# Optimization experiments

Hardware: AMD Instinct MI355X
Metric: run time of the kernel (lower is better)

Reference implementation:

```python
import jax, jax.numpy as jnp
import numpy as np

EPS = 1e-8


def setup_inputs() -> dict:
    key = jax.random.key(0)
    kx, kw, kb = jax.random.split(key, 3)
    B, S, K, N = 64, 4096, 256, 256
    x = jax.random.normal(kx, (B, S, K), dtype=jnp.float32)
    # Kaiming-uniform-ish init for weight (out_features, in_features)
    bound_w = np.sqrt(6.0 / K) / np.sqrt(1.0 + 5.0)  # kaiming_uniform with a=sqrt(5)
    weight = jax.random.uniform(kw, (N, K), dtype=jnp.float32, minval=-bound_w, maxval=bound_w)
    bound_b = 1.0 / np.sqrt(K)
    bias = jax.random.uniform(kb, (N,), dtype=jnp.float32, minval=-bound_b, maxval=bound_b)
    return {"x": x, "weight": weight, "bias": bias}


def reference(x, weight, bias):
    """LNS inference path of LNSLinear.

    log_out[m, n] = logsumexp_k(log(|x[m,k]|+eps) + log(|w[n,k]|+eps))
    out = sign(sign(x) @ sign(w).T) * exp(log_out) + bias
    Computed stably as log(exp(lx - mx) @ exp(lw - mw).T) + mx + mw.
    """
    orig_shape = x.shape
    K = weight.shape[1]
    xf = x.reshape(-1, K)                                  # [M, K]
    log_x = jnp.log(jnp.abs(xf) + EPS)                     # [M, K]
    x_sign = jnp.sign(xf)                                  # [M, K]
    log_w = jnp.log(jnp.abs(weight) + EPS)                 # [N, K]
    w_sign = jnp.sign(weight)                              # [N, K]

    mx = jnp.max(log_x, axis=-1, keepdims=True)            # [M, 1]
    mw = jnp.max(log_w, axis=-1, keepdims=True)            # [N, 1]
    # logsumexp over k without materializing [M, N, K]
    acc = jnp.einsum('mk,nk->mn', jnp.exp(log_x - mx), jnp.exp(log_w - mw))
    log_out = jnp.log(acc) + mx + mw.T                     # [M, N]

    out_sign = jnp.sign(jnp.einsum('mk,nk->mn', x_sign, w_sign))
    out = out_sign * jnp.exp(log_out) + bias
    return out.reshape(orig_shape[:-1] + (weight.shape[0],))
```

## Files before the change

### kernel.cpp

```cpp
#include <hip/hip_runtime.h>
#include <stdint.h>


#define K_DIM 256
#define N_DIM 256
#define BM 64
#define BN 128
#define BK 32
#define NKBLK 8
#define AROW 72

typedef float f32x4 __attribute__((ext_vector_type(4)));
typedef __bf16 bf16x8 __attribute__((ext_vector_type(8)));
typedef unsigned short u16x4v __attribute__((ext_vector_type(4)));
typedef unsigned short u16x8v __attribute__((ext_vector_type(8)));
typedef unsigned int u32x4v __attribute__((ext_vector_type(4)));

__global__ void w_convert_kernel(const float* __restrict__ W, unsigned short* __restrict__ Wp) {
    int t = blockIdx.x * 256 + threadIdx.x;
    int n = t >> 6;
    int k = (t & 63) << 2;
    float4 v = *(const float4*)(W + (size_t)n * K_DIM + k);
    unsigned short* row = Wp + ((size_t)n * NKBLK + (k >> 5)) * 64;
    int pos = k & 31;
    float vv[4] = {v.x, v.y, v.z, v.w};
    u16x4v a, s;
#pragma unroll
    for (int j = 0; j < 4; ++j) {
        __bf16 h = (__bf16)__builtin_fabsf(vv[j]);
        a[j] = __builtin_bit_cast(unsigned short, h);
        unsigned int u = __float_as_uint(vv[j]);
        s[j] = (unsigned short)(0x3F80u | ((u >> 16) & 0x8000u));
    }
    *(u16x4v*)(row + pos) = a;
    *(u16x4v*)(row + 32 + pos) = s;
}

__device__ __forceinline__ void gload_lds16(const void* g, void* l) {
    __builtin_amdgcn_global_load_lds(
        (const __attribute__((address_space(1))) unsigned int*)g,
        (__attribute__((address_space(3))) unsigned int*)l, 16, 0, 0);
}

__device__ __forceinline__ unsigned int sgnpk(float hi, float lo) {
    return (__builtin_amdgcn_perm(__float_as_uint(hi), __float_as_uint(lo), 0x07000300u)
            & 0x80008000u) | 0x3F803F80u;
}

__global__ __launch_bounds__(256, 4)
void lns_gemm_kernel(const float* __restrict__ X, const unsigned short* __restrict__ Wp,
                     const float* __restrict__ bias, float* __restrict__ out) {
    __shared__ __attribute__((aligned(16))) unsigned short sA[2][BM * AROW];
    __shared__ __attribute__((aligned(16))) unsigned short sB[2][BN * 64];

    const int tid  = threadIdx.x;
    const int lane = tid & 63;
    const int wave = tid >> 6;
    const int quad = lane >> 4;
    const int l16  = lane & 15;
    const int mb   = blockIdx.y;
    const int nb   = blockIdx.x;
    const int wm   = (wave >> 1) * 32;
    const int wn   = (wave & 1) * 64;

    const int ar = tid >> 2;
    const int aq = tid & 3;
    const float* gA = X + (size_t)(mb * BM + ar) * K_DIM + aq * 8;
    unsigned short* const wA0 = &sA[0][ar * AROW + aq * 8];
    unsigned short* const wA1 = &sA[1][ar * AROW + aq * 8];

    const unsigned short* gB[4];
    int dstB[4];
#pragma unroll
    for (int i = 0; i < 4; ++i) {
        int f = i * 256 + tid;
        int r = f >> 3;
        int g = (f & 7) ^ (r & 7);
        gB[i] = Wp + ((size_t)(nb * BN + r)) * (NKBLK * 64) + g * 8;
        dstB[i] = (i * 256 + wave * 64) * 8;
    }

    f32x4 accP[2][4], accS[2][4];
#pragma unroll
    for (int i = 0; i < 2; ++i)
#pragma unroll
        for (int j = 0; j < 4; ++j) {
            accP[i][j] = (f32x4)(0.0f);
            accS[i][j] = (f32x4)(0.0f);
        }

    f32x4 ra[2];

#define LOAD_A(kbv) do { \
        const f32x4* _p = (const f32x4*)(gA + (kbv) * BK); \
        ra[0] = _p[0]; ra[1] = _p[1]; \
    } while (0)

#define CONV_WRITE_A(dst) do { \
        u16x8v _ab; \
        _Pragma("unroll") \
        for (int _j = 0; _j < 4; ++_j) { \
            _ab[_j]     = __builtin_bit_cast(unsigned short, (__bf16)__builtin_fabsf(ra[0][_j])); \
            _ab[_j + 4] = __builtin_bit_cast(unsigned short, (__bf16)__builtin_fabsf(ra[1][_j])); \
        } \
        u32x4v _sg; \
        _sg[0] = sgnpk(ra[0][1], ra[0][0]); _sg[1] = sgnpk(ra[0][3], ra[0][2]); \
        _sg[2] = sgnpk(ra[1][1], ra[1][0]); _sg[3] = sgnpk(ra[1][3], ra[1][2]); \
        *(u16x8v*)(dst)        = _ab; \
        *(u32x4v*)((dst) + 32) = _sg; \
    } while (0)

    LOAD_A(0);
#pragma unroll
    for (int i = 0; i < 4; ++i) gload_lds16(gB[i], &sB[0][dstB[i]]);
    asm volatile("s_waitcnt vmcnt(4)" ::: "memory");
    CONV_WRITE_A(wA0);
    LOAD_A(1);
#pragma unroll
    for (int i = 0; i < 4; ++i) gload_lds16(gB[i] + 64, &sB[1][dstB[i]]);
    asm volatile("s_waitcnt vmcnt(6) lgkmcnt(0)\n\ts_barrier" ::: "memory");

#pragma unroll
    for (int kb = 0; kb < NKBLK; ++kb) {
        const int cur = kb & 1;
        const int nxt = cur ^ 1;

        if (kb >= 1 && kb + 1 < NKBLK) {
#pragma unroll
            for (int i = 0; i < 4; ++i)
                gload_lds16(gB[i] + (kb + 1) * 64, &sB[nxt][dstB[i]]);
        }

        bf16x8 aab[2], asg[2];
#pragma unroll
        for (int mi = 0; mi < 2; ++mi) {
            const unsigned short* rp = &sA[cur][(wm + mi * 16 + l16) * AROW + quad * 8];
            aab[mi] = __builtin_bit_cast(bf16x8, *(const u16x8v*)rp);
            asg[mi] = __builtin_bit_cast(bf16x8, *(const u16x8v*)(rp + 32));
        }
#pragma unroll
        for (int ni = 0; ni < 4; ++ni) {
            int r = wn + ni * 16 + l16;
            const unsigned short* rp = &sB[cur][r * 64];
            int sa = quad ^ (r & 7);
            bf16x8 bab = __builtin_bit_cast(bf16x8, *(const u16x8v*)(rp + sa * 8));
            bf16x8 bsg = __builtin_bit_cast(bf16x8, *(const u16x8v*)(rp + (sa ^ 4) * 8));
            accP[0][ni] = __builtin_amdgcn_mfma_f32_16x16x32_bf16(aab[0], bab, accP[0][ni], 0, 0, 0);
            accP[1][ni] = __builtin_amdgcn_mfma_f32_16x16x32_bf16(aab[1], bab, accP[1][ni], 0, 0, 0);
            accS[0][ni] = __builtin_amdgcn_mfma_f32_16x16x32_bf16(asg[0], bsg, accS[0][ni], 0, 0, 0);
            accS[1][ni] = __builtin_amdgcn_mfma_f32_16x16x32_bf16(asg[1], bsg, accS[1][ni], 0, 0, 0);
        }

        if (kb + 1 < NKBLK) {
            asm volatile("s_waitcnt vmcnt(4)" ::: "memory");
            CONV_WRITE_A((kb & 1) ? wA0 : wA1);
        }
        if (kb + 2 < NKBLK) LOAD_A(kb + 2);
        if (kb + 1 < NKBLK) {
            if (kb + 2 < NKBLK)
                asm volatile("s_waitcnt vmcnt(2) lgkmcnt(0)\n\ts_barrier" ::: "memory");
            else
                asm volatile("s_waitcnt vmcnt(0) lgkmcnt(0)\n\ts_barrier" ::: "memory");
        }
    }

#pragma unroll
    for (int ni = 0; ni < 4; ++ni) {
        int n   = nb * BN + wn + ni * 16 + l16;
        float b = bias[n];
#pragma unroll
        for (int mi = 0; mi < 2; ++mi) {
            int mbase = mb * BM + wm + mi * 16 + quad * 4;
#pragma unroll
            for (int r = 0; r < 4; ++r) {
                float p = accP[mi][ni][r];
                float s = accS[mi][ni][r];
                float v = (s > 0.0f) ? p : ((s < 0.0f) ? -p : 0.0f);
                out[(size_t)(mbase + r) * N_DIM + n] = v + b;
            }
        }
    }
}

extern "C" void kernel_launch(void* const* d_in, const int* in_sizes, int n_in,
                              void* d_out, int out_size, void* d_ws, size_t ws_size,
                              hipStream_t stream) {
    const float* x    = (const float*)d_in[0];
    const float* w    = (const float*)d_in[1];
    const float* bias = (const float*)d_in[2];
    float* out        = (float*)d_out;
    unsigned short* Wp = (unsigned short*)d_ws;

    const int M = in_sizes[0] / K_DIM;

    w_convert_kernel<<<dim3(64, 1, 1), dim3(256, 1, 1), 0, stream>>>(w, Wp);

    dim3 grid(N_DIM / BN, M / BM, 1);
    dim3 block(256, 1, 1);
    lns_gemm_kernel<<<grid, block, 0, stream>>>(x, Wp, bias, out);
}
```

Baseline: 486.6 us.

## Store signed bf16 in LDS and unpack abs/sign in registers

Shared-memory tiles now hold a single signed bf16 value per element instead of separate abs and sign copies. The abs and sign operands are derived in registers with bit masks just before the MFMAs. This halves LDS footprint and W traffic, uses an XOR swizzle in place of padding, and raises launch bounds occupancy to 5. The cost is extra VALU mask work in the inner loop and different waitcnt counts that must stay correct.

```diff
diff --git a/kernel.cpp b/kernel.cpp
--- a/kernel.cpp
+++ b/kernel.cpp
@@ -8,7 +8,6 @@
 #define BN 128
 #define BK 32
 #define NKBLK 8
-#define AROW 72
 
 typedef float f32x4 __attribute__((ext_vector_type(4)));
 typedef __bf16 bf16x8 __attribute__((ext_vector_type(8)));
@@ -18,22 +17,13 @@
 
 __global__ void w_convert_kernel(const float* __restrict__ W, unsigned short* __restrict__ Wp) {
     int t = blockIdx.x * 256 + threadIdx.x;
-    int n = t >> 6;
-    int k = (t & 63) << 2;
-    float4 v = *(const float4*)(W + (size_t)n * K_DIM + k);
-    unsigned short* row = Wp + ((size_t)n * NKBLK + (k >> 5)) * 64;
-    int pos = k & 31;
+    float4 v = *(const float4*)(W + (size_t)t * 4);
     float vv[4] = {v.x, v.y, v.z, v.w};
-    u16x4v a, s;
+    u16x4v o;
 #pragma unroll
-    for (int j = 0; j < 4; ++j) {
-        __bf16 h = (__bf16)__builtin_fabsf(vv[j]);
-        a[j] = __builtin_bit_cast(unsigned short, h);
-        unsigned int u = __float_as_uint(vv[j]);
-        s[j] = (unsigned short)(0x3F80u | ((u >> 16) & 0x8000u));
-    }
-    *(u16x4v*)(row + pos) = a;
-    *(u16x4v*)(row + 32 + pos) = s;
+    for (int j = 0; j < 4; ++j)
+        o[j] = __builtin_bit_cast(unsigned short, (__bf16)vv[j]);
+    *(u16x4v*)(Wp + (size_t)t * 4) = o;
 }
 
 __device__ __forceinline__ void gload_lds16(const void* g, void* l) {
@@ -42,16 +32,23 @@
         (__attribute__((address_space(3))) unsigned int*)l, 16, 0, 0);
 }
 
-__device__ __forceinline__ unsigned int sgnpk(float hi, float lo) {
-    return (__builtin_amdgcn_perm(__float_as_uint(hi), __float_as_uint(lo), 0x07000300u)
-            & 0x80008000u) | 0x3F803F80u;
+__device__ __forceinline__ void unpack_abs_sgn(const unsigned short* rp, bf16x8& ab, bf16x8& sg) {
+    u32x4v v = *(const u32x4v*)rp;
+    u32x4v a, s;
+#pragma unroll
+    for (int j = 0; j < 4; ++j) {
+        a[j] = v[j] & 0x7FFF7FFFu;
+        s[j] = (v[j] & 0x80008000u) | 0x3F803F80u;
+    }
+    ab = __builtin_bit_cast(bf16x8, a);
+    sg = __builtin_bit_cast(bf16x8, s);
 }
 
-__global__ __launch_bounds__(256, 4)
+__global__ __launch_bounds__(256, 5)
 void lns_gemm_kernel(const float* __restrict__ X, const unsigned short* __restrict__ Wp,
                      const float* __restrict__ bias, float* __restrict__ out) {
-    __shared__ __attribute__((aligned(16))) unsigned short sA[2][BM * AROW];
-    __shared__ __attribute__((aligned(16))) unsigned short sB[2][BN * 64];
+    __shared__ __attribute__((aligned(16))) unsigned short sA[2][BM * 32];
+    __shared__ __attribute__((aligned(16))) unsigned short sB[2][BN * 32];
 
     const int tid  = threadIdx.x;
     const int lane = tid & 63;
@@ -66,17 +63,18 @@
     const int ar = tid >> 2;
     const int aq = tid & 3;
     const float* gA = X + (size_t)(mb * BM + ar) * K_DIM + aq * 8;
-    unsigned short* const wA0 = &sA[0][ar * AROW + aq * 8];
-    unsigned short* const wA1 = &sA[1][ar * AROW + aq * 8];
+    const int aslot = aq ^ (ar & 3);
+    unsigned short* const wA0 = &sA[0][ar * 32 + aslot * 8];
+    unsigned short* const wA1 = &sA[1][ar * 32 + aslot * 8];
 
-    const unsigned short* gB[4];
-    int dstB[4];
+    const unsigned short* gB[2];
+    int dstB[2];
 #pragma unroll
-    for (int i = 0; i < 4; ++i) {
+    for (int i = 0; i < 2; ++i) {
         int f = i * 256 + tid;
-        int r = f >> 3;
-        int g = (f & 7) ^ (r & 7);
-        gB[i] = Wp + ((size_t)(nb * BN + r)) * (NKBLK * 64) + g * 8;
+        int r = f >> 2;
+        int g = (f & 3) ^ (r & 3);
+        gB[i] = Wp + (size_t)(nb * BN + r) * K_DIM + g * 8;
         dstB[i] = (i * 256 + wave * 64) * 8;
     }
 
@@ -97,28 +95,24 @@
     } while (0)
 
 #define CONV_WRITE_A(dst) do { \
-        u16x8v _ab; \
+        u16x8v _v; \
         _Pragma("unroll") \
         for (int _j = 0; _j < 4; ++_j) { \
-            _ab[_j]     = __builtin_bit_cast(unsigned short, (__bf16)__builtin_fabsf(ra[0][_j])); \
-            _ab[_j + 4] = __builtin_bit_cast(unsigned short, (__bf16)__builtin_fabsf(ra[1][_j])); \
+            _v[_j]     = __builtin_bit_cast(unsigned short, (__bf16)ra[0][_j]); \
+            _v[_j + 4] = __builtin_bit_cast(unsigned short, (__bf16)ra[1][_j]); \
         } \
-        u32x4v _sg; \
-        _sg[0] = sgnpk(ra[0][1], ra[0][0]); _sg[1] = sgnpk(ra[0][3], ra[0][2]); \
-        _sg[2] = sgnpk(ra[1][1], ra[1][0]); _sg[3] = sgnpk(ra[1][3], ra[1][2]); \
-        *(u16x8v*)(dst)        = _ab; \
-        *(u32x4v*)((dst) + 32) = _sg; \
+        *(u16x8v*)(dst) = _v; \
     } while (0)
 
     LOAD_A(0);
 #pragma unroll
-    for (int i = 0; i < 4; ++i) gload_lds16(gB[i], &sB[0][dstB[i]]);
-    asm volatile("s_waitcnt vmcnt(4)" ::: "memory");
+    for (int i = 0; i < 2; ++i) gload_lds16(gB[i], &sB[0][dstB[i]]);
+    asm volatile("s_waitcnt vmcnt(2)" ::: "memory");
     CONV_WRITE_A(wA0);
     LOAD_A(1);
 #pragma unroll
-    for (int i = 0; i < 4; ++i) gload_lds16(gB[i] + 64, &sB[1][dstB[i]]);
-    asm volatile("s_waitcnt vmcnt(6) lgkmcnt(0)\n\ts_barrier" ::: "memory");
+    for (int i = 0; i < 2; ++i) gload_lds16(gB[i] + 32, &sB[1][dstB[i]]);
+    asm volatile("s_waitcnt vmcnt(4) lgkmcnt(0)\n\ts_barrier" ::: "memory");
 
 #pragma unroll
     for (int kb = 0; kb < NKBLK; ++kb) {
@@ -127,24 +121,21 @@
 
         if (kb >= 1 && kb + 1 < NKBLK) {
 #pragma unroll
-            for (int i = 0; i < 4; ++i)
-                gload_lds16(gB[i] + (kb + 1) * 64, &sB[nxt][dstB[i]]);
+            for (int i = 0; i < 2; ++i)
+                gload_lds16(gB[i] + (kb + 1) * 32, &sB[nxt][dstB[i]]);
         }
 
         bf16x8 aab[2], asg[2];
 #pragma unroll
         for (int mi = 0; mi < 2; ++mi) {
-            const unsigned short* rp = &sA[cur][(wm + mi * 16 + l16) * AROW + quad * 8];
-            aab[mi] = __builtin_bit_cast(bf16x8, *(const u16x8v*)rp);
-            asg[mi] = __builtin_bit_cast(bf16x8, *(const u16x8v*)(rp + 32));
+            int m = wm + mi * 16 + l16;
+            unpack_abs_sgn(&sA[cur][m * 32 + (quad ^ (m & 3)) * 8], aab[mi], asg[mi]);
         }
 #pragma unroll
         for (int ni = 0; ni < 4; ++ni) {
             int r = wn + ni * 16 + l16;
-            const unsigned short* rp = &sB[cur][r * 64];
-            int sa = quad ^ (r & 7);
-            bf16x8 bab = __builtin_bit_cast(bf16x8, *(const u16x8v*)(rp + sa * 8));
-            bf16x8 bsg = __builtin_bit_cast(bf16x8, *(const u16x8v*)(rp + (sa ^ 4) * 8));
+            bf16x8 bab, bsg;
+            unpack_abs_sgn(&sB[cur][r * 32 + (quad ^ (r & 3)) * 8], bab, bsg);
             accP[0][ni] = __builtin_amdgcn_mfma_f32_16x16x32_bf16(aab[0], bab, accP[0][ni], 0, 0, 0);
             accP[1][ni] = __builtin_amdgcn_mfma_f32_16x16x32_bf16(aab[1], bab, accP[1][ni], 0, 0, 0);
             accS[0][ni] = __builtin_amdgcn_mfma_f32_16x16x32_bf16(asg[0], bsg, accS[0][ni], 0, 0, 0);
@@ -152,7 +143,7 @@
         }
 
         if (kb + 1 < NKBLK) {
-            asm volatile("s_waitcnt vmcnt(4)" ::: "memory");
+            asm volatile("s_waitcnt vmcnt(2)" ::: "memory");
             CONV_WRITE_A((kb & 1) ? wA0 : wA1);
         }
         if (kb + 2 < NKBLK) LOAD_A(kb + 2);
```

After: 1.037 ms. 2.13x slower.

## Drop LDS staging; load A and B fragments directly from global into registers

Applied to the files above, without the earlier changes.

Removes shared-memory tiles and barriers. Each wave now loads its X rows straight into registers and converts them in place, and reads W fragments directly from global memory in planar abs and sign layouts. The block tile changes to 128x64, with each wave owning 32 rows across all 64 columns, and occupancy is relaxed to 3 blocks per SIMD. This avoids LDS writes and reads and the barrier stalls. In exchange, every wave fetches the weight data redundantly from global or L2, with no reuse across waves, and X columns are read by four grid blocks instead of two.

```diff
diff --git a/kernel.cpp b/kernel.cpp
--- a/kernel.cpp
+++ b/kernel.cpp
@@ -4,11 +4,7 @@
 
 #define K_DIM 256
 #define N_DIM 256
-#define BM 64
-#define BN 128
-#define BK 32
-#define NKBLK 8
-#define AROW 72
+#define PLANE (N_DIM * K_DIM)
 
 typedef float f32x4 __attribute__((ext_vector_type(4)));
 typedef __bf16 bf16x8 __attribute__((ext_vector_type(8)));
@@ -18,28 +14,17 @@
 
 __global__ void w_convert_kernel(const float* __restrict__ W, unsigned short* __restrict__ Wp) {
     int t = blockIdx.x * 256 + threadIdx.x;
-    int n = t >> 6;
-    int k = (t & 63) << 2;
-    float4 v = *(const float4*)(W + (size_t)n * K_DIM + k);
-    unsigned short* row = Wp + ((size_t)n * NKBLK + (k >> 5)) * 64;
-    int pos = k & 31;
+    float4 v = *(const float4*)(W + (size_t)t * 4);
     float vv[4] = {v.x, v.y, v.z, v.w};
     u16x4v a, s;
 #pragma unroll
     for (int j = 0; j < 4; ++j) {
-        __bf16 h = (__bf16)__builtin_fabsf(vv[j]);
-        a[j] = __builtin_bit_cast(unsigned short, h);
+        a[j] = __builtin_bit_cast(unsigned short, (__bf16)__builtin_fabsf(vv[j]));
         unsigned int u = __float_as_uint(vv[j]);
         s[j] = (unsigned short)(0x3F80u | ((u >> 16) & 0x8000u));
     }
-    *(u16x4v*)(row + pos) = a;
-    *(u16x4v*)(row + 32 + pos) = s;
-}
-
-__device__ __forceinline__ void gload_lds16(const void* g, void* l) {
-    __builtin_amdgcn_global_load_lds(
-        (const __attribute__((address_space(1))) unsigned int*)g,
-        (__attribute__((address_space(3))) unsigned int*)l, 16, 0, 0);
+    *(u16x4v*)(Wp + (size_t)t * 4) = a;
+    *(u16x4v*)(Wp + PLANE + (size_t)t * 4) = s;
 }
 
 __device__ __forceinline__ unsigned int sgnpk(float hi, float lo) {
@@ -47,38 +32,21 @@
             & 0x80008000u) | 0x3F803F80u;
 }
 
-__global__ __launch_bounds__(256, 4)
+__global__ __launch_bounds__(256, 3)
 void lns_gemm_kernel(const float* __restrict__ X, const unsigned short* __restrict__ Wp,
                      const float* __restrict__ bias, float* __restrict__ out) {
-    __shared__ __attribute__((aligned(16))) unsigned short sA[2][BM * AROW];
-    __shared__ __attribute__((aligned(16))) unsigned short sB[2][BN * 64];
-
     const int tid  = threadIdx.x;
     const int lane = tid & 63;
     const int wave = tid >> 6;
     const int quad = lane >> 4;
     const int l16  = lane & 15;
-    const int mb   = blockIdx.y;
     const int nb   = blockIdx.x;
-    const int wm   = (wave >> 1) * 32;
-    const int wn   = (wave & 1) * 64;
+    const int mrow = blockIdx.y * 128 + wave * 32;
 
-    const int ar = tid >> 2;
-    const int aq = tid & 3;
-    const float* gA = X + (size_t)(mb * BM + ar) * K_DIM + aq * 8;
-    unsigned short* const wA0 = &sA[0][ar * AROW + aq * 8];
-    unsigned short* const wA1 = &sA[1][ar * AROW + aq * 8];
+    const float* gA0 = X + (size_t)(mrow + l16) * K_DIM + quad * 8;
+    const float* gA1 = gA0 + (size_t)16 * K_DIM;
 
-    const unsigned short* gB[4];
-    int dstB[4];
-#pragma unroll
-    for (int i = 0; i < 4; ++i) {
-        int f = i * 256 + tid;
-        int r = f >> 3;
-        int g = (f & 7) ^ (r & 7);
-        gB[i] = Wp + ((size_t)(nb * BN + r)) * (NKBLK * 64) + g * 8;
-        dstB[i] = (i * 256 + wave * 64) * 8;
-    }
+    const unsigned short* gB = Wp + (size_t)(nb * 64 + l16) * K_DIM + quad * 8;
 
     f32x4 accP[2][4], accS[2][4];
 #pragma unroll
@@ -89,88 +57,74 @@
             accS[i][j] = (f32x4)(0.0f);
         }
 
-    f32x4 ra[2];
+    f32x4 ra0[4], ra1[4];
 
-#define LOAD_A(kbv) do { \
-        const f32x4* _p = (const f32x4*)(gA + (kbv) * BK); \
-        ra[0] = _p[0]; ra[1] = _p[1]; \
+#define LOAD_A(buf, kbv) do { \
+        (buf)[0] = *(const f32x4*)(gA0 + (kbv) * 32); \
+        (buf)[1] = *(const f32x4*)(gA0 + (kbv) * 32 + 4); \
+        (buf)[2] = *(const f32x4*)(gA1 + (kbv) * 32); \
+        (buf)[3] = *(const f32x4*)(gA1 + (kbv) * 32 + 4); \
     } while (0)
 
-#define CONV_WRITE_A(dst) do { \
-        u16x8v _ab; \
+#define CONV_A(buf, aab, asg) do { \
         _Pragma("unroll") \
-        for (int _j = 0; _j < 4; ++_j) { \
-            _ab[_j]     = __builtin_bit_cast(unsigned short, (__bf16)__builtin_fabsf(ra[0][_j])); \
-            _ab[_j + 4] = __builtin_bit_cast(unsigned short, (__bf16)__builtin_fabsf(ra[1][_j])); \
+        for (int _mi = 0; _mi < 2; ++_mi) { \
+            u16x8v _ab; \
+            _Pragma("unroll") \
+            for (int _j = 0; _j < 4; ++_j) { \
+                _ab[_j]     = __builtin_bit_cast(unsigned short, (__bf16)__builtin_fabsf((buf)[2 * _mi][_j])); \
+                _ab[_j + 4] = __builtin_bit_cast(unsigned short, (__bf16)__builtin_fabsf((buf)[2 * _mi + 1][_j])); \
+            } \
+            u32x4v _sg; \
+            _sg[0] = sgnpk((buf)[2 * _mi][1],     (buf)[2 * _mi][0]); \
+            _sg[1] = sgnpk((buf)[2 * _mi][3],     (buf)[2 * _mi][2]); \
+            _sg[2] = sgnpk((buf)[2 * _mi + 1][1], (buf)[2 * _mi + 1][0]); \
+            _sg[3] = sgnpk((buf)[2 * _mi + 1][3], (buf)[2 * _mi + 1][2]); \
+            (aab)[_mi] = __builtin_bit_cast(bf16x8, _ab); \
+            (asg)[_mi] = __builtin_bit_cast(bf16x8, _sg); \
         } \
-        u32x4v _sg; \
-        _sg[0] = sgnpk(ra[0][1], ra[0][0]); _sg[1] = sgnpk(ra[0][3], ra[0][2]); \
-        _sg[2] = sgnpk(ra[1][1], ra[1][0]); _sg[3] = sgnpk(ra[1][3], ra[1][2]); \
-        *(u16x8v*)(dst)        = _ab; \
-        *(u32x4v*)((dst) + 32) = _sg; \
     } while (0)
 
-    LOAD_A(0);
-#pragma unroll
-    for (int i = 0; i < 4; ++i) gload_lds16(gB[i], &sB[0][dstB[i]]);
-    asm volatile("s_waitcnt vmcnt(4)" ::: "memory");
-    CONV_WRITE_A(wA0);
-    LOAD_A(1);
-#pragma unroll
-    for (int i = 0; i < 4; ++i) gload_lds16(gB[i] + 64, &sB[1][dstB[i]]);
-    asm volatile("s_waitcnt vmcnt(6) lgkmcnt(0)\n\ts_barrier" ::: "memory");
+    LOAD_A(ra0, 0);
+    LOAD_A(ra1, 1);
 
 #pragma unroll
-    for (int kb = 0; kb < NKBLK; ++kb) {
-        const int cur = kb & 1;
-        const int nxt = cur ^ 1;
-
-        if (kb >= 1 && kb + 1 < NKBLK) {
+    for (int kb = 0; kb < 8; ++kb) {
+        u16x8v bb_ab[4], bb_sg[4];
 #pragma unroll
-            for (int i = 0; i < 4; ++i)
-                gload_lds16(gB[i] + (kb + 1) * 64, &sB[nxt][dstB[i]]);
+        for (int ni = 0; ni < 4; ++ni) {
+            const unsigned short* bp = gB + (size_t)ni * 16 * K_DIM + kb * 32;
+            bb_ab[ni] = *(const u16x8v*)bp;
+            bb_sg[ni] = *(const u16x8v*)(bp + PLANE);
         }
 
         bf16x8 aab[2], asg[2];
-#pragma unroll
-        for (int mi = 0; mi < 2; ++mi) {
-            const unsigned short* rp = &sA[cur][(wm + mi * 16 + l16) * AROW + quad * 8];
-            aab[mi] = __builtin_bit_cast(bf16x8, *(const u16x8v*)rp);
-            asg[mi] = __builtin_bit_cast(bf16x8, *(const u16x8v*)(rp + 32));
+        if ((kb & 1) == 0) CONV_A(ra0, aab, asg);
+        else               CONV_A(ra1, aab, asg);
+
+        if (kb + 2 < 8) {
+            if ((kb & 1) == 0) LOAD_A(ra0, kb + 2);
+            else               LOAD_A(ra1, kb + 2);
         }
+
 #pragma unroll
         for (int ni = 0; ni < 4; ++ni) {
-            int r = wn + ni * 16 + l16;
-            const unsigned short* rp = &sB[cur][r * 64];
-            int sa = quad ^ (r & 7);
-            bf16x8 bab = __builtin_bit_cast(bf16x8, *(const u16x8v*)(rp + sa * 8));
-            bf16x8 bsg = __builtin_bit_cast(bf16x8, *(const u16x8v*)(rp + (sa ^ 4) * 8));
+            bf16x8 bab = __builtin_bit_cast(bf16x8, bb_ab[ni]);
+            bf16x8 bsg = __builtin_bit_cast(bf16x8, bb_sg[ni]);
             accP[0][ni] = __builtin_amdgcn_mfma_f32_16x16x32_bf16(aab[0], bab, accP[0][ni], 0, 0, 0);
             accP[1][ni] = __builtin_amdgcn_mfma_f32_16x16x32_bf16(aab[1], bab, accP[1][ni], 0, 0, 0);
             accS[0][ni] = __builtin_amdgcn_mfma_f32_16x16x32_bf16(asg[0], bsg, accS[0][ni], 0, 0, 0);
             accS[1][ni] = __builtin_amdgcn_mfma_f32_16x16x32_bf16(asg[1], bsg, accS[1][ni], 0, 0, 0);
         }
-
-        if (kb + 1 < NKBLK) {
-            asm volatile("s_waitcnt vmcnt(4)" ::: "memory");
-            CONV_WRITE_A((kb & 1) ? wA0 : wA1);
-        }
-        if (kb + 2 < NKBLK) LOAD_A(kb + 2);
-        if (kb + 1 < NKBLK) {
-            if (kb + 2 < NKBLK)
-                asm volatile("s_waitcnt vmcnt(2) lgkmcnt(0)\n\ts_barrier" ::: "memory");
-            else
-                asm volatile("s_waitcnt vmcnt(0) lgkmcnt(0)\n\ts_barrier" ::: "memory");
-        }
     }
 
 #pragma unroll
     for (int ni = 0; ni < 4; ++ni) {
-        int n   = nb * BN + wn + ni * 16 + l16;
+        int n   = nb * 64 + ni * 16 + l16;
         float b = bias[n];
 #pragma unroll
         for (int mi = 0; mi < 2; ++mi) {
-            int mbase = mb * BM + wm + mi * 16 + quad * 4;
+            int mbase = mrow + mi * 16 + quad * 4;
 #pragma unroll
             for (int r = 0; r < 4; ++r) {
                 float p = accP[mi][ni][r];
@@ -195,7 +149,7 @@
 
     w_convert_kernel<<<dim3(64, 1, 1), dim3(256, 1, 1), 0, stream>>>(w, Wp);
 
-    dim3 grid(N_DIM / BN, M / BM, 1);
+    dim3 grid(N_DIM / 64, M / 128, 1);
     dim3 block(256, 1, 1);
     lns_gemm_kernel<<<grid, block, 0, stream>>>(x, Wp, bias, out);
 }
```

Measured after the change: 705.4 us. +45.0%, slower.
